# Kernel optimization log

Hardware: AMD Instinct MI355X
Metric: run time of the kernel (lower is better)

Reference implementation:

```python
import jax, jax.numpy as jnp
import numpy as np

S = 20  # amino-acid alphabet size (hardcoded in the layer)
EPS = 1e-16


def setup_inputs() -> dict:
    key = jax.random.key(0)
    k1, k2, k3, k4, k5 = jax.random.split(key, 5)
    m, b, L, k = 2, 256, 1024, 8
    return {
        "sequences": jax.random.uniform(k1, (m, b, L, S), dtype=jnp.float32),
        "exchangeability_kernel": jax.random.normal(k2, (m, k, S, S), dtype=jnp.float32),
        "equilibrium_kernel": jax.random.normal(k3, (m, k, S), dtype=jnp.float32),
        "tau_kernel": jax.random.normal(k4, (m, b), dtype=jnp.float32),
        "per_matrix_rates_kernel": jax.random.normal(k5, (m, k), dtype=jnp.float32),
    }


def _anc_probs(sequences, exch_kernel, eq_kernel, tau_kernel, pmr_kernel):
    eye = jnp.eye(S, dtype=sequences.dtype)
    # make_R: symmetrize, softplus, zero diagonal -> exchangeabilities (m,k,s,s)
    K = 0.5 * (exch_kernel + jnp.swapaxes(exch_kernel, -1, -2))
    R = jax.nn.softplus(K) * (1.0 - eye)
    # make_p: equilibrium distribution via softmax (m,k,s)
    p = jax.nn.softmax(eq_kernel, axis=-1)
    # make_rate_matrix: Q_ij = R_ij * p_j, diag = -rowsum, normalize to 1 sub/site
    Q = R * p[..., None, :]
    row = jnp.sum(Q, axis=-1)                      # (m,k,s)
    Q = Q - row[..., None] * eye
    mue = jnp.sum(p * row, axis=-1)                # (m,k) expected rate
    Q = Q / jnp.maximum(mue, EPS)[..., None, None]
    # branch lengths: softplus, per-matrix rates: softplus -> tau (m,b,k)
    tau = jax.nn.softplus(tau_kernel)              # (m,b)
    rho = jax.nn.softplus(pmr_kernel)              # (m,k)
    tau_mbk = tau[:, :, None] * rho[:, None, :]    # (m,b,k)
    # GTR expm via symmetrization: S_sym = D^{1/2} Q D^{-1/2} (symmetric)
    sp = jnp.sqrt(p)                               # (m,k,s)
    isp = 1.0 / sp
    Ssym = sp[..., :, None] * Q * isp[..., None, :]
    Ssym = 0.5 * (Ssym + jnp.swapaxes(Ssym, -1, -2))
    lam, U = jnp.linalg.eigh(Ssym)                 # (m,k,s), (m,k,s,s)
    E = jnp.exp(tau_mbk[..., None] * lam[:, None, :, :])  # (m,b,k,s)
    # P = D^{-1/2} U exp(tau*Lam) U^T D^{1/2}  -> (m,b,k,s,s)
    P = jnp.einsum('mkie,mbke,mkje->mbkij', U, E, U)
    P = isp[:, None, :, :, None] * P * sp[:, None, :, None, :]
    # prob lookup for vector-format sequences (not transposed)
    return jnp.einsum('mblz,mbkzs->mblks', sequences, P)


def reference(sequences, exchangeability_kernel, equilibrium_kernel, tau_kernel, per_matrix_rates_kernel):
    return _anc_probs(sequences, exchangeability_kernel, equilibrium_kernel,
                      tau_kernel, per_matrix_rates_kernel)
```

## Files before the change

kernel.cpp:

```cpp
#include <hip/hip_runtime.h>

#define AS 20
#define ASS 400
#define KK 8
#define BB 256
#define MM 2
#define LL 1024
#define NPOW 12

typedef float nfloat4 __attribute__((ext_vector_type(4)));

__device__ __forceinline__ float softplus_f(float x) {
    return x > 20.f ? x : log1pf(expf(x));
}

__device__ __forceinline__ void wsync() {
    __builtin_amdgcn_sched_barrier(0);
    asm volatile("s_waitcnt lgkmcnt(0)" ::: "memory");
    __builtin_amdgcn_sched_barrier(0);
}

__device__ __forceinline__ void mul20w(const float* __restrict__ A,
                                       const float* __restrict__ B,
                                       float* __restrict__ C, int lane) {
    wsync();
    if (lane < 50) {
        const int i2 = (lane / 5) * 2;
        const int c4 = (lane % 5) * 4;
        float a0[AS], a1[AS];
        #pragma unroll
        for (int q = 0; q < 5; q++) {
            float4 v0 = *(const float4*)&A[i2 * AS + 4 * q];
            float4 v1 = *(const float4*)&A[(i2 + 1) * AS + 4 * q];
            a0[4*q] = v0.x; a0[4*q+1] = v0.y; a0[4*q+2] = v0.z; a0[4*q+3] = v0.w;
            a1[4*q] = v1.x; a1[4*q+1] = v1.y; a1[4*q+2] = v1.z; a1[4*q+3] = v1.w;
        }
        float4 s0 = {0.f,0.f,0.f,0.f}, s1 = {0.f,0.f,0.f,0.f};
        #pragma unroll
        for (int z = 0; z < AS; z++) {
            float4 bv = *(const float4*)&B[z * AS + c4];
            s0.x = fmaf(a0[z], bv.x, s0.x); s0.y = fmaf(a0[z], bv.y, s0.y);
            s0.z = fmaf(a0[z], bv.z, s0.z); s0.w = fmaf(a0[z], bv.w, s0.w);
            s1.x = fmaf(a1[z], bv.x, s1.x); s1.y = fmaf(a1[z], bv.y, s1.y);
            s1.z = fmaf(a1[z], bv.z, s1.z); s1.w = fmaf(a1[z], bv.w, s1.w);
        }
        *(float4*)&C[i2 * AS + c4] = s0;
        *(float4*)&C[(i2 + 1) * AS + c4] = s1;
    }
}

__global__ __launch_bounds__(256) void prep_powers_par(
    const float* __restrict__ exch, const float* __restrict__ eqk,
    const float* __restrict__ pmr,
    float* __restrict__ Spow_g,
    float* __restrict__ sp_g, float* __restrict__ isp_g,
    float* __restrict__ rho_g, float* __restrict__ nrm_g)
{
    const int mk = blockIdx.x;
    const int t = threadIdx.x;
    const int w = t >> 6, lane = t & 63;
    __shared__ float p[AS], sp[AS], isp[AS], rowsum[AS], rowabs[AS];
    __shared__ __align__(16) float SL[NPOW * ASS];

    const float* Km = exch + (size_t)mk * ASS;
    const float* ev = eqk + (size_t)mk * AS;

    if (t < AS) {
        float mx = -1e30f;
        for (int i = 0; i < AS; i++) mx = fmaxf(mx, ev[i]);
        float sum = 0.f;
        for (int i = 0; i < AS; i++) sum += expf(ev[i] - mx);
        float pl = expf(ev[t] - mx) / sum;
        p[t] = pl;
        float sq = sqrtf(pl);
        sp[t] = sq; isp[t] = 1.0f / sq;
    }
    if (t == 0) rho_g[mk] = softplus_f(pmr[mk]);
    __syncthreads();

    float* RP   = SL + ASS;
    float* RawS = SL + 2 * ASS;
    for (int f = t; f < ASS; f += 256) {
        int i = f / AS, j = f % AS;
        float Kv = 0.5f * (Km[i*AS+j] + Km[j*AS+i]);
        float Rv = (i == j) ? 0.f : softplus_f(Kv);
        RP[f] = Rv * p[j];
    }
    __syncthreads();
    if (t < AS) {
        float r = 0.f;
        for (int j = 0; j < AS; j++) r += RP[t*AS+j];
        rowsum[t] = r;
    }
    __syncthreads();
    float mue = 0.f;
    for (int i = 0; i < AS; i++) mue += p[i] * rowsum[i];
    const float inv_mue = 1.0f / fmaxf(mue, 1e-16f);
    for (int f = t; f < ASS; f += 256) {
        int i = f / AS, j = f % AS;
        float Qv = (RP[f] - (i == j ? rowsum[i] : 0.f)) * inv_mue;
        RawS[f] = sp[i] * Qv * isp[j];
    }
    __syncthreads();
    for (int f = t; f < ASS; f += 256) {
        int i = f / AS, j = f % AS;
        SL[f] = 0.5f * (RawS[f] + RawS[j*AS+i]);
    }
    __syncthreads();
    if (t < AS) {
        float r = 0.f;
        for (int j = 0; j < AS; j++) r += fabsf(SL[t*AS+j]);
        rowabs[t] = r;
    }
    __syncthreads();
    if (t == 0) {
        float n = 0.f;
        for (int i = 0; i < AS; i++) n = fmaxf(n, rowabs[i]);
        nrm_g[mk] = n;
    }
    if (t < AS) { sp_g[mk*AS + t] = sp[t]; isp_g[mk*AS + t] = isp[t]; }

    if (w == 0) mul20w(SL, SL, SL + ASS, lane);
    __syncthreads();
    if (w == 0) mul20w(SL + ASS, SL,       SL + 2*ASS, lane);
    if (w == 1) mul20w(SL + ASS, SL + ASS, SL + 3*ASS, lane);
    __syncthreads();
    if (w == 0) mul20w(SL + 3*ASS, SL,         SL + 4*ASS, lane);
    if (w == 1) mul20w(SL + 3*ASS, SL + ASS,   SL + 5*ASS, lane);
    if (w == 2) mul20w(SL + 3*ASS, SL + 2*ASS, SL + 6*ASS, lane);
    if (w == 3) mul20w(SL + 3*ASS, SL + 3*ASS, SL + 7*ASS, lane);
    __syncthreads();
    if (w == 0) mul20w(SL + 7*ASS, SL,         SL + 8*ASS, lane);
    if (w == 1) mul20w(SL + 7*ASS, SL + ASS,   SL + 9*ASS, lane);
    if (w == 2) mul20w(SL + 7*ASS, SL + 2*ASS, SL + 10*ASS, lane);
    if (w == 3) mul20w(SL + 7*ASS, SL + 3*ASS, SL + 11*ASS, lane);
    __syncthreads();

    float* Sg = Spow_g + (size_t)mk * NPOW * ASS;
    for (int f = t; f < NPOW * ASS; f += 256) Sg[f] = SL[f];
}

#define ACC4(A, Sv, Z) \
    A.x = fmaf(Sv, Preg[Z].x, A.x); A.y = fmaf(Sv, Preg[Z].y, A.y); \
    A.z = fmaf(Sv, Preg[Z].z, A.z); A.w = fmaf(Sv, Preg[Z].w, A.w);

__device__ __forceinline__ void nt_store4(float4 v, float* p) {
    nfloat4 nv; nv.x = v.x; nv.y = v.y; nv.z = v.z; nv.w = v.w;
    __builtin_nontemporal_store(nv, (nfloat4*)p);
}

__global__ __launch_bounds__(320, 4) void fused_apply(
    const float* __restrict__ seq, const float* __restrict__ Spow_g,
    const float* __restrict__ sp_g, const float* __restrict__ isp_g,
    const float* __restrict__ rho_g, const float* __restrict__ nrm_g,
    const float* __restrict__ tauk, float* __restrict__ out)
{
    const int blk = blockIdx.x;
    const int mb = blk >> 1;
    const int half = blk & 1;
    const int mi = mb / BB;
    const int t = threadIdx.x;
    const int w = t >> 6;
    const int lane = t & 63;

    __shared__ __align__(16) float Plds[KK * ASS];
    __shared__ __align__(16) float4 sbuf[2][320];
    __shared__ float coefs[KK][NPOW];
    __shared__ float spk[KK * AS], ispk[KK * AS];
    __shared__ float scs[KK];
    __shared__ int ssh[KK];

    float* Tmp = (float*)sbuf;

    const int rowbase = half * (LL / 2);
    const float* seqb = seq + (size_t)mb * LL * AS;
    float* outb = out + (size_t)mb * LL * (KK * AS);

    const float4 first = ((const float4*)(seqb + (size_t)rowbase * AS))[t];

    if (t < KK) {
        const float tau = softplus_f(tauk[mb]) * rho_g[mi * KK + t];
        const float nt = tau * nrm_g[mi * KK + t];
        int s = 0;
        if (nt > 2.0f) {
            s = (int)ceilf(log2f(nt * 0.5f));
            if (s < 0) s = 0;
            if (s > 12) s = 12;
        }
        ssh[t] = s;
        scs[t] = ldexpf(tau, -s);
    }
    if (t < KK * AS) {
        spk[t]  = sp_g [mi * KK * AS + t];
        ispk[t] = isp_g[mi * KK * AS + t];
    }
    __syncthreads();
    if (t < KK * NPOW) {
        const int k = t / NPOW, n = t % NPOW + 1;
        const float sc = scs[k];
        float scp = sc, fact = 1.f;
        for (int q = 2; q <= n; ++q) { scp *= sc; fact *= (float)q; }
        coefs[k][n - 1] = scp / fact;
    }
    __syncthreads();

    {
        const float* Sbase = Spow_g + (size_t)mi * KK * NPOW * ASS;
        #pragma unroll 2
        for (int e = t; e < KK * ASS; e += 320) {
            const int k = e / ASS;
            const int f = e - k * ASS;
            const int i = f / AS, jj = f - i * AS;
            const float* Sg = Sbase + (size_t)k * NPOW * ASS + f;
            float acc = (i == jj) ? 1.f : 0.f;
            #pragma unroll
            for (int n = 1; n <= NPOW; ++n)
                acc = fmaf(coefs[k][n - 1], Sg[(n - 1) * ASS], acc);
            Plds[e] = acc;
        }
    }
    __syncthreads();

    {
        const int nk = (w < 3) ? 2 : 1;
        for (int pi = 0; pi < nk; ++pi) {
            const int k = (pi == 0) ? w : w + 5;
            const int s = ssh[k];
            float* Pk = &Plds[k * ASS];
            float* Tw = &Tmp[w * ASS];
            for (int q = 0; q < s; ++q) {
                if ((q & 1) == 0) mul20w(Pk, Pk, Tw, lane);
                else              mul20w(Tw, Tw, Pk, lane);
            }
            if (s & 1) {
                wsync();
                if (lane < 50) {
                    #pragma unroll
                    for (int u = 0; u < 8; ++u) Pk[lane * 8 + u] = Tw[lane * 8 + u];
                }
            }
        }
    }
    __syncthreads();

    for (int e = t; e < KK * ASS; e += 320) {
        const int k = e / ASS;
        const int f = e - k * ASS;
        const int i = f / AS, jj = f - i * AS;
        Plds[e] *= ispk[k * AS + i] * spk[k * AS + jj];
    }
    __syncthreads();

    const int j = t % 40;
    const int rg = t / 40;
    const int ki = j / 5;
    const int s0 = (j % 5) * 4;

    float4 Preg[AS];
    #pragma unroll
    for (int z = 0; z < AS; z++)
        Preg[z] = *(const float4*)&Plds[ki * ASS + z * AS + s0];
    __syncthreads();
    sbuf[0][t] = first;
    __syncthreads();

    float* stbase = outb + (size_t)rowbase * 160 + t * 4;

    for (int c = 0; c < 8; c++) {
        const int cur = c & 1;
        float4 rnext;
        if (c < 7)
            rnext = ((const float4*)(seqb + (size_t)(rowbase + (c + 1) * 64) * AS))[t];
        float* stc = stbase + (size_t)c * 64 * 160;
        #pragma unroll
        for (int pp = 0; pp < 4; pp++) {
            const int lrA = rg + 16 * pp;
            const int lrB = lrA + 8;
            const float4* rowA = &sbuf[cur][lrA * 5];
            const float4* rowB = &sbuf[cur][lrB * 5];
            float4 a0 = {0.f,0.f,0.f,0.f}, a1 = {0.f,0.f,0.f,0.f};
            #pragma unroll
            for (int q = 0; q < 5; q++) {
                float4 svA = rowA[q];
                float4 svB = rowB[q];
                ACC4(a0, svA.x, 4*q+0)  ACC4(a1, svB.x, 4*q+0)
                ACC4(a0, svA.y, 4*q+1)  ACC4(a1, svB.y, 4*q+1)
                ACC4(a0, svA.z, 4*q+2)  ACC4(a1, svB.z, 4*q+2)
                ACC4(a0, svA.w, 4*q+3)  ACC4(a1, svB.w, 4*q+3)
            }
            nt_store4(a0, stc + pp * 2560);
            nt_store4(a1, stc + pp * 2560 + 1280);
        }
        if (c < 7) sbuf[cur ^ 1][t] = rnext;
        __syncthreads();
    }
}

extern "C" void kernel_launch(void* const* d_in, const int* in_sizes, int n_in,
                              void* d_out, int out_size, void* d_ws, size_t ws_size,
                              hipStream_t stream) {
    const float* seq  = (const float*)d_in[0];
    const float* exch = (const float*)d_in[1];
    const float* eqk  = (const float*)d_in[2];
    const float* tauk = (const float*)d_in[3];
    const float* pmr  = (const float*)d_in[4];
    float* out = (float*)d_out;

    float* ws   = (float*)d_ws;
    float* Spow = ws;
    float* spg  = Spow + (size_t)MM * KK * NPOW * ASS;
    float* ispg = spg + MM * KK * AS;
    float* rhog = ispg + MM * KK * AS;
    float* nrmg = rhog + MM * KK;

    prep_powers_par<<<dim3(MM * KK), dim3(256), 0, stream>>>(
        exch, eqk, pmr, Spow, spg, ispg, rhog, nrmg);
    fused_apply<<<dim3(MM * BB * 2), dim3(320), 0, stream>>>(
        seq, Spow, spg, ispg, rhog, nrmg, tauk, out);
}
```

Baseline: 106.0 us.

## Compute sequence-by-P lookup with bf16 MFMA instead of FP32 FMAs

Replaces the per-thread FP32 FMA loop that multiplies each 20-wide sequence row by the per-matrix P columns with two 32x32x16 bf16 MFMA instructions per 32-row tile. Sequences and P are rounded to bf16 and staged in a padded LDS tile, with the K dimension zero-padded from 20 to 32. Output is written as scalar nontemporal stores rather than float4 stores. The goal is to cut ALU time in the apply loop, at the cost of reduced precision from bf16 inputs and narrower, strided store patterns.

```diff
diff --git a/kernel.cpp b/kernel.cpp
--- a/kernel.cpp
+++ b/kernel.cpp
@@ -8,7 +8,14 @@
 #define LL 1024
 #define NPOW 12
 
-typedef float nfloat4 __attribute__((ext_vector_type(4)));
+typedef __attribute__((ext_vector_type(8))) short bf16x8;
+typedef __attribute__((ext_vector_type(16))) float f32x16;
+
+__device__ __forceinline__ unsigned short f2bf(float x) {
+    unsigned int u = __builtin_bit_cast(unsigned int, x);
+    u += 0x7FFFu + ((u >> 16) & 1u);
+    return (unsigned short)(u >> 16);
+}
 
 __device__ __forceinline__ float softplus_f(float x) {
     return x > 20.f ? x : log1pf(expf(x));
@@ -140,15 +147,6 @@
     for (int f = t; f < NPOW * ASS; f += 256) Sg[f] = SL[f];
 }
 
-#define ACC4(A, Sv, Z) \
-    A.x = fmaf(Sv, Preg[Z].x, A.x); A.y = fmaf(Sv, Preg[Z].y, A.y); \
-    A.z = fmaf(Sv, Preg[Z].z, A.z); A.w = fmaf(Sv, Preg[Z].w, A.w);
-
-__device__ __forceinline__ void nt_store4(float4 v, float* p) {
-    nfloat4 nv; nv.x = v.x; nv.y = v.y; nv.z = v.z; nv.w = v.w;
-    __builtin_nontemporal_store(nv, (nfloat4*)p);
-}
-
 __global__ __launch_bounds__(320, 4) void fused_apply(
     const float* __restrict__ seq, const float* __restrict__ Spow_g,
     const float* __restrict__ sp_g, const float* __restrict__ isp_g,
@@ -163,14 +161,14 @@
     const int w = t >> 6;
     const int lane = t & 63;
 
-    __shared__ __align__(16) float Plds[KK * ASS];
-    __shared__ __align__(16) float4 sbuf[2][320];
+    __shared__ __align__(16) float regionA[KK * ASS];
+    __shared__ __align__(16) float Tmp[5 * ASS];
     __shared__ float coefs[KK][NPOW];
     __shared__ float spk[KK * AS], ispk[KK * AS];
     __shared__ float scs[KK];
     __shared__ int ssh[KK];
 
-    float* Tmp = (float*)sbuf;
+    float* Plds = regionA;
 
     const int rowbase = half * (LL / 2);
     const float* seqb = seq + (size_t)mb * LL * AS;
@@ -251,47 +249,65 @@
     }
     __syncthreads();
 
-    const int j = t % 40;
-    const int rg = t / 40;
-    const int ki = j / 5;
-    const int s0 = (j % 5) * 4;
-
-    float4 Preg[AS];
+    const int mycol = w * 32 + (lane & 31);
+    const int bki = mycol / 20, bs = mycol % 20;
+    const float* Pcol = Plds + bki * ASS + bs;
+    bf16x8 bf0, bf1;
     #pragma unroll
-    for (int z = 0; z < AS; z++)
-        Preg[z] = *(const float4*)&Plds[ki * ASS + z * AS + s0];
-    __syncthreads();
-    sbuf[0][t] = first;
-    __syncthreads();
-
-    float* stbase = outb + (size_t)rowbase * 160 + t * 4;
-
-    for (int c = 0; c < 8; c++) {
+    for (int jj = 0; jj < 8; ++jj) {
+        const int k0 = (lane >> 5) * 8 + jj;
+        const int k1 = 16 + k0;
+        bf0[jj] = (short)f2bf(Pcol[k0 * AS]);
+        bf1[jj] = (k1 < AS) ? (short)f2bf(Pcol[k1 * AS]) : (short)0;
+    }
+    __syncthreads();
+
+    unsigned short* tile = (unsigned short*)regionA;
+    for (int i = t; i < 384; i += 320) {
+        const int b = i / 192, r = (i % 192) / 3, q = i % 3;
+        *(uint2*)((char*)tile + b * 5120 + r * 80 + 40 + q * 8) = make_uint2(0u, 0u);
+    }
+    {
+        const int r = t / 5, pc = t % 5;
+        const unsigned int lo = (unsigned)f2bf(first.x) | ((unsigned)f2bf(first.y) << 16);
+        const unsigned int hi = (unsigned)f2bf(first.z) | ((unsigned)f2bf(first.w) << 16);
+        *(uint2*)((char*)tile + r * 80 + pc * 8) = make_uint2(lo, hi);
+    }
+    __syncthreads();
+
+    for (int c = 0; c < 8; ++c) {
         const int cur = c & 1;
         float4 rnext;
         if (c < 7)
             rnext = ((const float4*)(seqb + (size_t)(rowbase + (c + 1) * 64) * AS))[t];
-        float* stc = stbase + (size_t)c * 64 * 160;
+
+        const char* tb = (const char*)tile + cur * 5120;
+        float* chout = outb + (size_t)(rowbase + c * 64) * 160;
+
         #pragma unroll
-        for (int pp = 0; pp < 4; pp++) {
-            const int lrA = rg + 16 * pp;
-            const int lrB = lrA + 8;
-            const float4* rowA = &sbuf[cur][lrA * 5];
-            const float4* rowB = &sbuf[cur][lrB * 5];
-            float4 a0 = {0.f,0.f,0.f,0.f}, a1 = {0.f,0.f,0.f,0.f};
+        for (int tr = 0; tr < 2; ++tr) {
+            const char* arow = tb + (tr * 32 + (lane & 31)) * 80 + (lane >> 5) * 16;
+            const bf16x8 a0 = *(const bf16x8*)(arow);
+            const bf16x8 a1 = *(const bf16x8*)(arow + 32);
+            f32x16 d = {0.f,0.f,0.f,0.f,0.f,0.f,0.f,0.f,
+                        0.f,0.f,0.f,0.f,0.f,0.f,0.f,0.f};
+            d = __builtin_amdgcn_mfma_f32_32x32x16_bf16(a0, bf0, d, 0, 0, 0);
+            d = __builtin_amdgcn_mfma_f32_32x32x16_bf16(a1, bf1, d, 0, 0, 0);
+            float* sb = chout + (size_t)(tr * 32 + (lane >> 5) * 4) * 160
+                        + w * 32 + (lane & 31);
             #pragma unroll
-            for (int q = 0; q < 5; q++) {
-                float4 svA = rowA[q];
-                float4 svB = rowB[q];
-                ACC4(a0, svA.x, 4*q+0)  ACC4(a1, svB.x, 4*q+0)
-                ACC4(a0, svA.y, 4*q+1)  ACC4(a1, svB.y, 4*q+1)
-                ACC4(a0, svA.z, 4*q+2)  ACC4(a1, svB.z, 4*q+2)
-                ACC4(a0, svA.w, 4*q+3)  ACC4(a1, svB.w, 4*q+3)
+            for (int r = 0; r < 16; ++r) {
+                const int rl = (r & 3) + 8 * (r >> 2);
+                __builtin_nontemporal_store(d[r], sb + rl * 160);
             }
-            nt_store4(a0, stc + pp * 2560);
-            nt_store4(a1, stc + pp * 2560 + 1280);
-        }
-        if (c < 7) sbuf[cur ^ 1][t] = rnext;
+        }
+
+        if (c < 7) {
+            const int r = t / 5, pc = t % 5;
+            const unsigned int lo = (unsigned)f2bf(rnext.x) | ((unsigned)f2bf(rnext.y) << 16);
+            const unsigned int hi = (unsigned)f2bf(rnext.z) | ((unsigned)f2bf(rnext.w) << 16);
+            *(uint2*)((char*)tile + (cur ^ 1) * 5120 + r * 80 + pc * 8) = make_uint2(lo, hi);
+        }
         __syncthreads();
     }
 }
```

Result: faster. 85.61 us (-19.2%).
